# Kernel optimization log

Measured on AMD Instinct MI355X. Metric: run time of the kernel, lower is better.

The kernel has to match this reference:

```python
import jax, jax.numpy as jnp
import numpy as np

B = 16384
N_HIDDEN_TYPE = 16   # n_hidden option count (first block of output columns)
N_ACTIVE_TYPE = 8
N_OUT = N_HIDDEN_TYPE + N_ACTIVE_TYPE   # 24, also LSTM input size
H = 24                                   # LSTM hidden size (hardcoded in module)
LAYER_LIMIT = 24
STEPS = 2 * LAYER_LIMIT - 1              # 47


def setup_inputs() -> dict:
    key = jax.random.key(0)
    ks = jax.random.split(key, 7)
    s = 0.1
    return {
        "W_ih": jax.random.normal(ks[0], (4 * H, N_OUT), jnp.float32) * s,
        "W_hh": jax.random.normal(ks[1], (4 * H, H), jnp.float32) * s,
        "b_ih": jax.random.normal(ks[2], (4 * H,), jnp.float32) * s,
        "b_hh": jax.random.normal(ks[3], (4 * H,), jnp.float32) * s,
        "Wl": jax.random.normal(ks[4], (N_OUT, H), jnp.float32) * s,
        "bl": jax.random.normal(ks[5], (N_OUT,), jnp.float32) * s,
        "rand": jax.random.uniform(ks[6], (STEPS, B), jnp.float32),
    }


def reference(W_ih, W_hh, b_ih, b_hh, Wl, bl, rand):
    cols = jnp.arange(N_OUT)

    def step(carry, xs):
        h, c, a = carry
        i, r = xs  # i: step index (scalar), r: (B,) uniforms
        # PyTorch LSTMCell: gate order input, forget, cell, output
        gates = a @ W_ih.T + b_ih + h @ W_hh.T + b_hh
        ig, fg, gg, og = jnp.split(gates, 4, axis=1)
        c = jax.nn.sigmoid(fg) * c + jax.nn.sigmoid(ig) * jnp.tanh(gg)
        h = jax.nn.sigmoid(og) * jnp.tanh(c)
        logits = h @ Wl.T + bl  # (B, N_OUT)
        counter = (i + 1) // 2  # counter_nb_layers at an odd step
        mask = jnp.where(i % 2 == 1, cols < counter, cols >= N_HIDDEN_TYPE)
        p = jax.nn.softmax(jnp.where(mask, logits, -jnp.inf), axis=1)
        # stochastic sampling: first index where cumsum exceeds uniform
        act = jnp.argmax(jnp.cumsum(p, axis=1) > r[:, None], axis=1)
        pr = jnp.take_along_axis(p, act[:, None], axis=1)[:, 0]
        a_next = jax.nn.one_hot(act, N_OUT, dtype=logits.dtype)
        return (h, c, a_next), (pr, act)

    h0 = jnp.zeros((B, H), jnp.float32)
    c0 = jnp.zeros((B, H), jnp.float32)
    a0 = jnp.zeros((B, N_OUT), jnp.float32)
    _, (prob, actions) = jax.lax.scan(
        step, (h0, c0, a0), (jnp.arange(STEPS), rand))
    # stack over time -> (B, STEPS), actions as float like the numpy array
    return prob.T, actions.T.astype(jnp.float32)
```

## Files before the change

kernel.cpp:

```cpp
#include <hip/hip_runtime.h>
#include <math.h>

#define BATCH   16384
#define HD      24
#define NOUTC   24
#define NHID    16
#define NSTEPS  47
#define NG      96
#define GRP     16
#define NTG     12
#define JPW     2
#define GPW     8
#define THREADS 192

typedef float v2f __attribute__((ext_vector_type(2)));
union F4 { float4 v; v2f h[2]; float f[4]; };

__device__ __forceinline__ v2f pk_fma(v2f a, v2f b, v2f c) {
    v2f d;
    asm("v_pk_fma_f32 %0, %1, %2, %3" : "=v"(d) : "v"(a), "v"(b), "v"(c));
    return d;
}

__device__ __forceinline__ float fast_sigmoid(float x) {
    float t = __expf(-x);
    return __builtin_amdgcn_rcpf(1.0f + t);
}
__device__ __forceinline__ float fast_tanh(float x) {
    float ax = fabsf(x);
    float t  = __expf(-2.0f * ax);
    float r  = (1.0f - t) * __builtin_amdgcn_rcpf(1.0f + t);
    return copysignf(r, x);
}

template <int T>
__device__ __forceinline__ void finish_odd(const float* sLrow, int cnt, float r,
                                           int& a, float& pr) {
    float v[T];
    #pragma unroll
    for (int n4 = 0; n4 < T / 4; ++n4) {
        F4 vv; vv.v = *(const float4*)&sLrow[n4 * 4];
        v[n4 * 4 + 0] = vv.f[0]; v[n4 * 4 + 1] = vv.f[1];
        v[n4 * 4 + 2] = vv.f[2]; v[n4 * 4 + 3] = vv.f[3];
    }
    float t[T];
    #pragma unroll
    for (int n = 0; n < T; ++n) t[n] = (n < cnt) ? v[n] : -INFINITY;
    #pragma unroll
    for (int stride = T / 2; stride >= 1; stride >>= 1)
        #pragma unroll
        for (int n = 0; n < stride; ++n) t[n] = fmaxf(t[n], t[n + stride]);
    const float m = t[0];
    float e_[T];
    #pragma unroll
    for (int n = 0; n < T; ++n) e_[n] = (n < cnt) ? __expf(v[n] - m) : 0.f;
    float c[T];
    float run = 0.f;
    #pragma unroll
    for (int n = 0; n < T; ++n) { run += e_[n]; c[n] = run; }
    const float Z  = c[T - 1];
    const float rZ = r * Z;
    bool found = false;
    float ea = 0.f;
    a = 0;
    #pragma unroll
    for (int n = 0; n < T; ++n) {
        if (!found && c[n] > rZ) { found = true; a = n; ea = e_[n]; }
    }
    if (!found) { a = 0; ea = e_[0]; }
    pr = ea / Z;
}

__global__ __launch_bounds__(THREADS, 3) void policy_kernel(
    const float* __restrict__ W_ih, const float* __restrict__ W_hh,
    const float* __restrict__ b_ih, const float* __restrict__ b_hh,
    const float* __restrict__ Wl,   const float* __restrict__ bl,
    const float* __restrict__ rnd,  float* __restrict__ out)
{
    __shared__ float sWihB[NG][25];
    __shared__ float sBias[NG];
    __shared__ __align__(16) float sWhhP[HD][NTG][GPW];
    __shared__ __align__(8)  float sWlP[HD][NTG][JPW];
    __shared__ float sBl[NOUTC];
    __shared__ __align__(16) float hhT[GRP][28];
    __shared__ __align__(16) float sLt[GRP][28];
    __shared__ float sPr[GRP][NSTEPS + 1];
    __shared__ unsigned char sAct8[GRP][NSTEPS + 1];
    __shared__ int sActCur[GRP];

    const int tid = threadIdx.x;
    const int w   = tid >> 4;
    const int e   = tid & 15;
    const int wv  = tid >> 6;
    const int b   = blockIdx.x * GRP + e;

    for (int i = tid; i < NG * HD; i += THREADS) {
        int g = i / HD, k = i % HD;
        float bs = b_ih[g] + b_hh[g];
        sWihB[g][k] = W_ih[i] + bs;
        int t = g / 24, rem = g % 24;
        sWhhP[k][rem >> 1][t * JPW + (rem & 1)] = W_hh[i];
    }
    for (int i = tid; i < NOUTC * HD; i += THREADS) {
        int n = i / HD, k = i % HD;
        sWlP[k][n >> 1][n & 1] = Wl[i];
    }
    if (tid < NG)    sBias[tid] = b_ih[tid] + b_hh[tid];
    if (tid < NOUTC) sBl[tid]   = bl[tid];
    __syncthreads();

    float cst[JPW] = {0.f, 0.f};
    {
        float h0, h1;
        #pragma unroll
        for (int i = 0; i < JPW; ++i) {
            float g0 = sBias[0 * 24 + w * JPW + i];
            float g1 = sBias[1 * 24 + w * JPW + i];
            float g2 = sBias[2 * 24 + w * JPW + i];
            float g3 = sBias[3 * 24 + w * JPW + i];
            float si = fast_sigmoid(g0);
            float sf = fast_sigmoid(g1);
            float tg = fast_tanh(g2);
            float so = fast_sigmoid(g3);
            float cj = sf * cst[i] + si * tg;
            cst[i] = cj;
            float hv = so * fast_tanh(cj);
            if (i == 0) h0 = hv; else h1 = hv;
        }
        *(float2*)&hhT[e][2 * w] = make_float2(h0, h1);
    }

    float r_cur = 0.f;
    if (w == 0) r_cur = rnd[b];
    __syncthreads();

    v2f aN[4];

    for (int s = 0; s < NSTEPS; ++s) {
        const int  cnt = (s + 1) >> 1;
        const bool odd = (s & 1) != 0;

        const bool doLog = odd ? (8 * wv < cnt) : (wv == 2);
        if (doLog) {
            v2f aL = (v2f){0.f, 0.f};
            #pragma unroll
            for (int c = 0; c < 6; ++c) {
                F4 hx; hx.v = *(const float4*)&hhT[e][c * 4];
                #pragma unroll
                for (int q = 0; q < 4; ++q) {
                    int k = c * 4 + q;
                    v2f hk2; hk2.x = hx.f[q]; hk2.y = hx.f[q];
                    v2f lv = *(const v2f*)&sWlP[k][w][0];
                    aL = pk_fma(hk2, lv, aL);
                }
            }
            sLt[e][w * JPW + 0] = aL.x + sBl[w * JPW + 0];
            sLt[e][w * JPW + 1] = aL.y + sBl[w * JPW + 1];
        }
        __syncthreads();

        if (w == 0) {
            const float r = r_cur;
            int a;
            float pr;
            if (odd) {
                if (cnt <= 8)       finish_odd<8 >(&sLt[e][0], cnt, r, a, pr);
                else if (cnt <= 16) finish_odd<16>(&sLt[e][0], cnt, r, a, pr);
                else                finish_odd<24>(&sLt[e][0], cnt, r, a, pr);
            } else {
                float v8[8];
                {
                    F4 x0, x1;
                    x0.v = *(const float4*)&sLt[e][16];
                    x1.v = *(const float4*)&sLt[e][20];
                    #pragma unroll
                    for (int i = 0; i < 4; ++i) { v8[i] = x0.f[i]; v8[4 + i] = x1.f[i]; }
                }
                float t4[8];
                #pragma unroll
                for (int i = 0; i < 8; ++i) t4[i] = v8[i];
                #pragma unroll
                for (int stride = 4; stride >= 1; stride >>= 1)
                    #pragma unroll
                    for (int i = 0; i < stride; ++i) t4[i] = fmaxf(t4[i], t4[i + stride]);
                const float m = t4[0];
                float e8[8], c8[8];
                #pragma unroll
                for (int i = 0; i < 8; ++i) e8[i] = __expf(v8[i] - m);
                float run = 0.f;
                #pragma unroll
                for (int i = 0; i < 8; ++i) { run += e8[i]; c8[i] = run; }
                const float Z  = c8[7];
                const float rZ = r * Z;
                bool found = false;
                float ea = 0.f;
                int a2 = 0;
                #pragma unroll
                for (int i = 0; i < 8; ++i) {
                    if (!found && c8[i] > rZ) { found = true; a2 = NHID + i; ea = e8[i]; }
                }
                if (!found) { a2 = 0; ea = 0.f; }
                a  = a2;
                pr = ea / Z;
            }
            sPr[e][s]   = pr;
            sAct8[e][s] = (unsigned char)a;
            sActCur[e]  = a;
            r_cur = rnd[((s + 1 < NSTEPS) ? (s + 1) : s) * BATCH + b];
        }

        #pragma unroll
        for (int q = 0; q < 4; ++q) aN[q] = (v2f){0.f, 0.f};
        #pragma unroll 2
        for (int c = 0; c < 6; ++c) {
            F4 hx; hx.v = *(const float4*)&hhT[e][c * 4];
            #pragma unroll
            for (int q = 0; q < 4; ++q) {
                int k = c * 4 + q;
                v2f hk2; hk2.x = hx.f[q]; hk2.y = hx.f[q];
                const float* wp = &sWhhP[k][w][0];
                F4 u0, u1;
                u0.v = *(const float4*)&wp[0];
                u1.v = *(const float4*)&wp[4];
                aN[0] = pk_fma(hk2, u0.h[0], aN[0]);
                aN[1] = pk_fma(hk2, u0.h[1], aN[1]);
                aN[2] = pk_fma(hk2, u1.h[0], aN[2]);
                aN[3] = pk_fma(hk2, u1.h[1], aN[3]);
            }
        }
        __syncthreads();

        {
            const int actE = sActCur[e];
            float h0, h1;
            #pragma unroll
            for (int i = 0; i < JPW; ++i) {
                float g0 = ((i == 0) ? aN[0].x : aN[0].y) + sWihB[0 * 24 + w * JPW + i][actE];
                float g1 = ((i == 0) ? aN[1].x : aN[1].y) + sWihB[1 * 24 + w * JPW + i][actE];
                float g2 = ((i == 0) ? aN[2].x : aN[2].y) + sWihB[2 * 24 + w * JPW + i][actE];
                float g3 = ((i == 0) ? aN[3].x : aN[3].y) + sWihB[3 * 24 + w * JPW + i][actE];
                float si = fast_sigmoid(g0);
                float sf = fast_sigmoid(g1);
                float tg = fast_tanh(g2);
                float so = fast_sigmoid(g3);
                float cj = sf * cst[i] + si * tg;
                cst[i] = cj;
                float hv = so * fast_tanh(cj);
                if (i == 0) h0 = hv; else h1 = hv;
            }
            *(float2*)&hhT[e][2 * w] = make_float2(h0, h1);
        }
        __syncthreads();
    }

    const int base = blockIdx.x * GRP * NSTEPS;
    for (int i = tid; i < GRP * NSTEPS; i += THREADS) {
        int rr = i / NSTEPS, ss = i - rr * NSTEPS;
        out[base + i]                          = sPr[rr][ss];
        out[(size_t)BATCH * NSTEPS + base + i] = (float)sAct8[rr][ss];
    }
}

extern "C" void kernel_launch(void* const* d_in, const int* in_sizes, int n_in,
                              void* d_out, int out_size, void* d_ws, size_t ws_size,
                              hipStream_t stream) {
    const float* W_ih = (const float*)d_in[0];
    const float* W_hh = (const float*)d_in[1];
    const float* b_ih = (const float*)d_in[2];
    const float* b_hh = (const float*)d_in[3];
    const float* Wl   = (const float*)d_in[4];
    const float* bl   = (const float*)d_in[5];
    const float* rnd  = (const float*)d_in[6];
    float* o = (float*)d_out;

    policy_kernel<<<BATCH / GRP, THREADS, 0, stream>>>(W_ih, W_hh, b_ih, b_hh, Wl, bl, rnd, o);
}
```

Baseline: 146.3 us.

## Compute sampling redundantly per wave via shuffles and double-buffer hidden state

For even steps and odd steps with at most 8 candidates, each 64-lane wave computes the 8 relevant logits itself and gathers them with cross-lane shuffles. Every thread then runs the softmax and sampling redundantly, so the chosen action stays in a register and no longer passes through shared memory. The hidden state is double-buffered by step parity, which removes two of the three block barriers per step on these steps; large odd steps still use shared memory and one extra barrier. The cost is redundant sampling work on every thread and extra shared-memory weight copies.

```diff
diff --git a/kernel.cpp b/kernel.cpp
--- a/kernel.cpp
+++ b/kernel.cpp
@@ -81,17 +81,18 @@
     __shared__ float sBias[NG];
     __shared__ __align__(16) float sWhhP[HD][NTG][GPW];
     __shared__ __align__(8)  float sWlP[HD][NTG][JPW];
+    __shared__ __align__(8)  float sWlPE[HD][4][JPW];
     __shared__ float sBl[NOUTC];
-    __shared__ __align__(16) float hhT[GRP][28];
+    __shared__ __align__(16) float hh[2][GRP][28];
     __shared__ __align__(16) float sLt[GRP][28];
     __shared__ float sPr[GRP][NSTEPS + 1];
     __shared__ unsigned char sAct8[GRP][NSTEPS + 1];
-    __shared__ int sActCur[GRP];
 
     const int tid = threadIdx.x;
     const int w   = tid >> 4;
     const int e   = tid & 15;
     const int wv  = tid >> 6;
+    const int wl  = w & 3;
     const int b   = blockIdx.x * GRP + e;
 
     for (int i = tid; i < NG * HD; i += THREADS) {
@@ -103,7 +104,9 @@
     }
     for (int i = tid; i < NOUTC * HD; i += THREADS) {
         int n = i / HD, k = i % HD;
-        sWlP[k][n >> 1][n & 1] = Wl[i];
+        float wlv = Wl[i];
+        sWlP[k][n >> 1][n & 1] = wlv;
+        if (n >= 16) sWlPE[k][(n - 16) >> 1][n & 1] = wlv;
     }
     if (tid < NG)    sBias[tid] = b_ih[tid] + b_hh[tid];
     if (tid < NOUTC) sBl[tid]   = bl[tid];
@@ -127,63 +130,104 @@
             float hv = so * fast_tanh(cj);
             if (i == 0) h0 = hv; else h1 = hv;
         }
-        *(float2*)&hhT[e][2 * w] = make_float2(h0, h1);
-    }
-
-    float r_cur = 0.f;
-    if (w == 0) r_cur = rnd[b];
+        *(float2*)&hh[0][e][2 * w] = make_float2(h0, h1);
+    }
+    float r_cur = rnd[b];
     __syncthreads();
 
     v2f aN[4];
 
     for (int s = 0; s < NSTEPS; ++s) {
-        const int  cnt = (s + 1) >> 1;
-        const bool odd = (s & 1) != 0;
-
-        const bool doLog = odd ? (8 * wv < cnt) : (wv == 2);
-        if (doLog) {
+        const int  cnt    = (s + 1) >> 1;
+        const bool odd    = (s & 1) != 0;
+        const bool bigOdd = odd && (cnt > 8);
+        const int  par    = s & 1;
+
+        float l0 = 0.f, l1 = 0.f;
+        if (bigOdd) {
+            if (8 * wv < cnt) {
+                v2f aL = (v2f){0.f, 0.f};
+                #pragma unroll
+                for (int c = 0; c < 6; ++c) {
+                    F4 hx; hx.v = *(const float4*)&hh[par][e][c * 4];
+                    #pragma unroll
+                    for (int q = 0; q < 4; ++q) {
+                        int k = c * 4 + q;
+                        v2f hk2; hk2.x = hx.f[q]; hk2.y = hx.f[q];
+                        v2f lv = *(const v2f*)&sWlP[k][w][0];
+                        aL = pk_fma(hk2, lv, aL);
+                    }
+                }
+                sLt[e][w * JPW + 0] = aL.x + sBl[w * JPW + 0];
+                sLt[e][w * JPW + 1] = aL.y + sBl[w * JPW + 1];
+            }
+            __syncthreads();
+        } else {
             v2f aL = (v2f){0.f, 0.f};
             #pragma unroll
             for (int c = 0; c < 6; ++c) {
-                F4 hx; hx.v = *(const float4*)&hhT[e][c * 4];
+                F4 hx; hx.v = *(const float4*)&hh[par][e][c * 4];
                 #pragma unroll
                 for (int q = 0; q < 4; ++q) {
                     int k = c * 4 + q;
                     v2f hk2; hk2.x = hx.f[q]; hk2.y = hx.f[q];
-                    v2f lv = *(const v2f*)&sWlP[k][w][0];
+                    v2f lv = odd ? *(const v2f*)&sWlP[k][wl][0]
+                                 : *(const v2f*)&sWlPE[k][wl][0];
                     aL = pk_fma(hk2, lv, aL);
                 }
             }
-            sLt[e][w * JPW + 0] = aL.x + sBl[w * JPW + 0];
-            sLt[e][w * JPW + 1] = aL.y + sBl[w * JPW + 1];
-        }
-        __syncthreads();
-
-        if (w == 0) {
-            const float r = r_cur;
-            int a;
-            float pr;
+            const int n0 = odd ? (2 * wl) : (16 + 2 * wl);
+            l0 = aL.x + sBl[n0 + 0];
+            l1 = aL.y + sBl[n0 + 1];
+        }
+
+        int a = 0;
+        float pr;
+        const float r = r_cur;
+        if (bigOdd) {
+            if (cnt <= 16) finish_odd<16>(&sLt[e][0], cnt, r, a, pr);
+            else           finish_odd<24>(&sLt[e][0], cnt, r, a, pr);
+        } else {
+            float v8[8];
+            #pragma unroll
+            for (int i = 0; i < 8; ++i) {
+                float sv = (i & 1) ? l1 : l0;
+                v8[i] = __shfl(sv, ((i >> 1) << 4) | e, 64);
+            }
             if (odd) {
-                if (cnt <= 8)       finish_odd<8 >(&sLt[e][0], cnt, r, a, pr);
-                else if (cnt <= 16) finish_odd<16>(&sLt[e][0], cnt, r, a, pr);
-                else                finish_odd<24>(&sLt[e][0], cnt, r, a, pr);
+                float t8[8];
+                #pragma unroll
+                for (int n = 0; n < 8; ++n) t8[n] = (n < cnt) ? v8[n] : -INFINITY;
+                #pragma unroll
+                for (int st = 4; st >= 1; st >>= 1)
+                    #pragma unroll
+                    for (int n = 0; n < st; ++n) t8[n] = fmaxf(t8[n], t8[n + st]);
+                const float m = t8[0];
+                float e8[8], c8[8];
+                #pragma unroll
+                for (int n = 0; n < 8; ++n) e8[n] = (n < cnt) ? __expf(v8[n] - m) : 0.f;
+                float run = 0.f;
+                #pragma unroll
+                for (int n = 0; n < 8; ++n) { run += e8[n]; c8[n] = run; }
+                const float Z  = c8[7];
+                const float rZ = r * Z;
+                bool found = false;
+                float ea = 0.f;
+                #pragma unroll
+                for (int n = 0; n < 8; ++n) {
+                    if (!found && c8[n] > rZ) { found = true; a = n; ea = e8[n]; }
+                }
+                if (!found) { a = 0; ea = e8[0]; }
+                pr = ea / Z;
             } else {
-                float v8[8];
-                {
-                    F4 x0, x1;
-                    x0.v = *(const float4*)&sLt[e][16];
-                    x1.v = *(const float4*)&sLt[e][20];
+                float t8[8];
+                #pragma unroll
+                for (int i = 0; i < 8; ++i) t8[i] = v8[i];
+                #pragma unroll
+                for (int st = 4; st >= 1; st >>= 1)
                     #pragma unroll
-                    for (int i = 0; i < 4; ++i) { v8[i] = x0.f[i]; v8[4 + i] = x1.f[i]; }
-                }
-                float t4[8];
-                #pragma unroll
-                for (int i = 0; i < 8; ++i) t4[i] = v8[i];
-                #pragma unroll
-                for (int stride = 4; stride >= 1; stride >>= 1)
-                    #pragma unroll
-                    for (int i = 0; i < stride; ++i) t4[i] = fmaxf(t4[i], t4[i + stride]);
-                const float m = t4[0];
+                    for (int i = 0; i < st; ++i) t8[i] = fmaxf(t8[i], t8[i + st]);
+                const float m = t8[0];
                 float e8[8], c8[8];
                 #pragma unroll
                 for (int i = 0; i < 8; ++i) e8[i] = __expf(v8[i] - m);
@@ -194,26 +238,22 @@
                 const float rZ = r * Z;
                 bool found = false;
                 float ea = 0.f;
-                int a2 = 0;
                 #pragma unroll
                 for (int i = 0; i < 8; ++i) {
-                    if (!found && c8[i] > rZ) { found = true; a2 = NHID + i; ea = e8[i]; }
+                    if (!found && c8[i] > rZ) { found = true; a = NHID + i; ea = e8[i]; }
                 }
-                if (!found) { a2 = 0; ea = 0.f; }
-                a  = a2;
+                if (!found) { a = 0; ea = 0.f; }
                 pr = ea / Z;
             }
-            sPr[e][s]   = pr;
-            sAct8[e][s] = (unsigned char)a;
-            sActCur[e]  = a;
-            r_cur = rnd[((s + 1 < NSTEPS) ? (s + 1) : s) * BATCH + b];
-        }
+        }
+        if (tid < GRP) { sPr[tid][s] = pr; sAct8[tid][s] = (unsigned char)a; }
+        r_cur = rnd[((s + 1 < NSTEPS) ? (s + 1) : s) * BATCH + b];
 
         #pragma unroll
         for (int q = 0; q < 4; ++q) aN[q] = (v2f){0.f, 0.f};
         #pragma unroll 2
         for (int c = 0; c < 6; ++c) {
-            F4 hx; hx.v = *(const float4*)&hhT[e][c * 4];
+            F4 hx; hx.v = *(const float4*)&hh[par][e][c * 4];
             #pragma unroll
             for (int q = 0; q < 4; ++q) {
                 int k = c * 4 + q;
@@ -228,17 +268,15 @@
                 aN[3] = pk_fma(hk2, u1.h[1], aN[3]);
             }
         }
-        __syncthreads();
 
         {
-            const int actE = sActCur[e];
             float h0, h1;
             #pragma unroll
             for (int i = 0; i < JPW; ++i) {
-                float g0 = ((i == 0) ? aN[0].x : aN[0].y) + sWihB[0 * 24 + w * JPW + i][actE];
-                float g1 = ((i == 0) ? aN[1].x : aN[1].y) + sWihB[1 * 24 + w * JPW + i][actE];
-                float g2 = ((i == 0) ? aN[2].x : aN[2].y) + sWihB[2 * 24 + w * JPW + i][actE];
-                float g3 = ((i == 0) ? aN[3].x : aN[3].y) + sWihB[3 * 24 + w * JPW + i][actE];
+                float g0 = ((i == 0) ? aN[0].x : aN[0].y) + sWihB[0 * 24 + w * JPW + i][a];
+                float g1 = ((i == 0) ? aN[1].x : aN[1].y) + sWihB[1 * 24 + w * JPW + i][a];
+                float g2 = ((i == 0) ? aN[2].x : aN[2].y) + sWihB[2 * 24 + w * JPW + i][a];
+                float g3 = ((i == 0) ? aN[3].x : aN[3].y) + sWihB[3 * 24 + w * JPW + i][a];
                 float si = fast_sigmoid(g0);
                 float sf = fast_sigmoid(g1);
                 float tg = fast_tanh(g2);
@@ -248,7 +286,7 @@
                 float hv = so * fast_tanh(cj);
                 if (i == 0) h0 = hv; else h1 = hv;
             }
-            *(float2*)&hhT[e][2 * w] = make_float2(h0, h1);
+            *(float2*)&hh[1 - par][e][2 * w] = make_float2(h0, h1);
         }
         __syncthreads();
     }
```

New measurement: 177.6 us. 1.21x slower.
